# Optimization experiments

Measured on AMD Instinct MI355X. Metric: run time of the kernel, lower is better.

## Reference

```python
import jax, jax.numpy as jnp
import numpy as np

N_LABELS = 48
L = N_LABELS + 2            # labels + stop + start
START = N_LABELS + 1
STOP = N_LABELS
NEG = -10000.0
B, T = 512, 1024


def setup_inputs() -> dict:
    key = jax.random.key(0)
    k1, k2, k3 = jax.random.split(key, 3)
    feats = jax.random.normal(k1, (B, T, L), dtype=jnp.float32)
    lens = jax.random.randint(k2, (B,), 1, T + 1, dtype=jnp.int32)
    transitions = jax.random.normal(k3, (L, L), dtype=jnp.float32)
    return {"feats": feats, "lens": lens, "transitions": transitions}


def reference(feats, lens, transitions):
    # Viterbi decode (module's forward). feats: [B, T, L]
    b, t, l = feats.shape
    vit0 = jnp.full((b, l), NEG, feats.dtype).at[:, START].set(0.0)

    def step(carry, logit):
        vit, c = carry                                   # vit [B,L], c [B]
        scores = vit[:, None, :] + transitions[None, :, :]   # [B, to, from]
        vt_max = scores.max(2)                           # [B, L]
        ptr = scores.argmax(2)                           # [B, L] backpointers
        vit_nxt = vt_max + logit
        vit_new = jnp.where((c > 0)[:, None], vit_nxt, vit)
        # add stop transition exactly when this is the last real timestep
        vit_new = vit_new + jnp.where((c == 1)[:, None], transitions[STOP][None, :], 0.0)
        return (vit_new, c - 1), ptr

    (vit, _), pointers = jax.lax.scan(step, (vit0, lens), jnp.swapaxes(feats, 0, 1))
    scores = vit.max(1)                                  # [B]
    idx = vit.argmax(1)                                  # [B]

    barange = jnp.arange(b)

    def back(i, ptr):
        ni = ptr[barange, i]
        return ni, ni

    _, back_seq = jax.lax.scan(back, idx, pointers, reverse=True)  # back_seq[t] = idx after ptr_t
    # original drops the earliest backtracked index (belongs to the virtual start step)
    paths = jnp.concatenate([back_seq[1:], idx[None]], axis=0).T   # [B, T]
    return scores, paths
```

## Files before the change

### kernel.cpp

```cpp
#include <hip/hip_runtime.h>

typedef unsigned char u8;

#define TT 1024
#define BB 512
#define LL 50
#define STOPI 48
#define STARTI 49
#define NEGV -10000.0f

#define PTR_OFF 4096

#define ROW_ADDS(ROWP, S, TRR)                                                 \
    {                                                                          \
        _Pragma("unroll")                                                      \
        for (int k_ = 0; k_ < 13; ++k_) {                                      \
            const float4 q_ = *(const float4*)((ROWP) + 4 * k_);               \
            const int j_ = 4 * k_;                                             \
            (S)[j_ + 0] = q_.x + (TRR)[j_ + 0];                                \
            (S)[j_ + 1] = q_.y + (TRR)[j_ + 1];                                \
            if (j_ + 2 < LL) (S)[j_ + 2] = q_.z + (TRR)[j_ + 2];               \
            if (j_ + 3 < LL) (S)[j_ + 3] = q_.w + (TRR)[j_ + 3];               \
        }                                                                      \
    }

#define MAX50(S, M)                                                            \
    {                                                                          \
        float r0_[17];                                                         \
        _Pragma("unroll")                                                      \
        for (int k_ = 0; k_ < 16; ++k_)                                        \
            r0_[k_] = fmaxf(fmaxf((S)[3*k_], (S)[3*k_+1]), (S)[3*k_+2]);       \
        r0_[16] = fmaxf((S)[48], (S)[49]);                                     \
        float r1_[6];                                                          \
        _Pragma("unroll")                                                      \
        for (int k_ = 0; k_ < 5; ++k_)                                         \
            r1_[k_] = fmaxf(fmaxf(r0_[3*k_], r0_[3*k_+1]), r0_[3*k_+2]);       \
        r1_[5] = fmaxf(r0_[15], r0_[16]);                                      \
        (M) = fmaxf(fmaxf(fmaxf(r1_[0], r1_[1]), r1_[2]),                      \
                    fmaxf(fmaxf(r1_[3], r1_[4]), r1_[5]));                     \
    }

#define ARGMAX50(S, BI)                                                        \
    {                                                                          \
        float b0_=-3.4e38f, b1_=-3.4e38f, b2_=-3.4e38f, b3_=-3.4e38f;          \
        int   i0_=0, i1_=13, i2_=26, i3_=39;                                   \
        _Pragma("unroll")                                                      \
        for (int j_=0;  j_<13; ++j_){ const float v_=(S)[j_]; if (v_>b0_){b0_=v_;i0_=j_;} } \
        _Pragma("unroll")                                                      \
        for (int j_=13; j_<26; ++j_){ const float v_=(S)[j_]; if (v_>b1_){b1_=v_;i1_=j_;} } \
        _Pragma("unroll")                                                      \
        for (int j_=26; j_<39; ++j_){ const float v_=(S)[j_]; if (v_>b2_){b2_=v_;i2_=j_;} } \
        _Pragma("unroll")                                                      \
        for (int j_=39; j_<50; ++j_){ const float v_=(S)[j_]; if (v_>b3_){b3_=v_;i3_=j_;} } \
        if (b1_>b0_){b0_=b1_;i0_=i1_;}                                         \
        if (b2_>b0_){b0_=b2_;i0_=i2_;}                                         \
        if (b3_>b0_){b0_=b3_;i0_=i3_;}                                         \
        (BI) = i0_;                                                            \
    }

#define PROCESS_GROUP(BASE)                                                    \
    {                                                                          \
        if (!have && (BASE) + 3 > len) {                                       \
            const float* rowp_ = &ring[len & 15][0];                           \
            float s_[LL];                                                      \
            ROW_ADDS(rowp_, s_, trr)                                           \
            ARGMAX50(s_, cidx)                                                 \
            have = true;                                                       \
        }                                                                      \
        unsigned pk_ = 0;                                                      \
        _Pragma("unroll 1")                                                    \
        for (int r_ = 0; r_ < 4; ++r_) {                                       \
            const int t_ = (BASE) + r_;                                        \
            int idx_;                                                          \
            if (t_ <= len) {                                                   \
                const float* rowp_ = &ring[t_ & 15][0];                        \
                float s_[LL];                                                  \
                ROW_ADDS(rowp_, s_, trr)                                       \
                ARGMAX50(s_, idx_)                                             \
            } else {                                                           \
                idx_ = cidx;                                                   \
            }                                                                  \
            pk_ |= (unsigned)idx_ << (8 * r_);                                 \
        }                                                                      \
        if (lane < LL) *(unsigned*)(pt + (BASE)) = pk_;                        \
    }

__global__ __launch_bounds__(192, 2) void viterbi_fused(
    const float* __restrict__ feats, const int* __restrict__ lens,
    const float* __restrict__ trans, float* __restrict__ out_scores,
    int* __restrict__ idx_ws, u8* __restrict__ ptr_ws)
{
    const int b    = blockIdx.x;
    const int tid  = threadIdx.x;
    const int lane = tid & 63;
    const int w    = __builtin_amdgcn_readfirstlane(tid >> 6);
    const int row  = (lane < LL) ? lane : (LL - 1);

    __shared__ float ring[16][64];

    float trr[LL];
#pragma unroll
    for (int j = 0; j < LL; ++j) trr[j] = trans[row * LL + j];
    const int len = lens[b];

    if (w == 0) {
        const float tr_stop = trans[STOPI * LL + row];
        float vit = (lane == STARTI) ? 0.0f : NEGV;
        const float* fb = feats + (size_t)b * (TT * LL);

        float f[8];
#pragma unroll
        for (int i = 0; i < 8; ++i) f[i] = fb[i * LL + row];

        for (int it = 0; it < 128; ++it) {
#pragma unroll
            for (int i = 0; i < 8; ++i) {
                const int t = (it << 3) + i;
                float* rowp = &ring[t & 15][0];
                if (t <= len) {
                    if (lane < LL) rowp[lane] = vit;
                }
                if (t < len) {
                    float s[LL];
                    ROW_ADDS(rowp, s, trr)
                    float m; MAX50(s, m)
                    float nv = m + f[i];
                    if (t == len - 1) nv += tr_stop;
                    vit = nv;
                    int tp = t + 8; if (tp > TT - 1) tp = TT - 1;
                    f[i] = fb[(size_t)tp * LL + row];
                }
            }
            asm volatile("s_waitcnt lgkmcnt(0)" ::: "memory");
            __builtin_amdgcn_s_barrier();
            asm volatile("" ::: "memory");
        }

        float m = -3.4e38f; int mi = 0;
#pragma unroll
        for (int j = 0; j < LL; ++j) {
            float sv = __int_as_float(__builtin_amdgcn_readlane(__float_as_int(vit), j));
            if (sv > m) { m = sv; mi = j; }
        }
        if (lane == 0) { out_scores[b] = m; idx_ws[b] = mi; }
    } else {
        u8* pt = ptr_ws + (size_t)b * (TT * LL) + (size_t)row * TT;
        int  cidx = 0;
        bool have = false;

        for (int it = 0; it < 128; ++it) {
            if (it > 0) {
                const int base = ((it - 1) << 3) + ((w - 1) << 2);
                PROCESS_GROUP(base)
            }
            asm volatile("s_waitcnt lgkmcnt(0)" ::: "memory");
            __builtin_amdgcn_s_barrier();
            asm volatile("" ::: "memory");
        }
        {
            const int base = (127 << 3) + ((w - 1) << 2);
            PROCESS_GROUP(base)
        }
    }
}

#define LSW(S, T) (((S) << 10) + ((T) ^ (((S) & 31) << 2)))

__global__ __launch_bounds__(64) void viterbi_bwd(
    const int* __restrict__ idx_ws, const u8* __restrict__ ptr_ws,
    float* __restrict__ out_paths)
{
    const int b = blockIdx.x;
    const int lane = threadIdx.x;

    __shared__ u8 lptr[TT * LL];
    __shared__ u8 maps[32 * LL];
    __shared__ int entries[33];

    {
        const unsigned* src = (const unsigned*)(ptr_ws + (size_t)b * TT * LL);
        unsigned* dst = (unsigned*)lptr;
        for (int i = lane; i < (TT * LL) / 4; i += 64) {
            const int to = i >> 8;
            const int t4 = i & 255;
            dst[(to << 8) + (t4 ^ (to & 31))] = src[i];
        }
    }
    __syncthreads();

    {
        int st[25], tt[25], cidx[25];
#pragma unroll
        for (int k = 0; k < 25; ++k) {
            int ww = k * 64 + lane;
            int c = ww / 50;
            int l = ww - c * 50;
            st[k] = l;
            tt[k] = c * 32 + 31;
            cidx[k] = c * 50 + l;
        }
        for (int j = 0; j < 32; ++j) {
#pragma unroll
            for (int k = 0; k < 25; ++k) {
                st[k] = lptr[LSW(st[k], tt[k])];
                tt[k] -= 1;
            }
        }
#pragma unroll
        for (int k = 0; k < 25; ++k) maps[cidx[k]] = (u8)st[k];
    }
    __syncthreads();

    const int idx = idx_ws[b];

    if (lane == 0) {
        int i = idx;
        for (int c = 31; c >= 0; --c) {
            entries[c + 1] = i;
            i = maps[c * 50 + i];
        }
        entries[0] = i;
    }
    __syncthreads();

    float* po = out_paths + (size_t)b * TT;
    if (lane < 32) {
        const int c = lane;
        int s = entries[c + 1];
        for (int j = 0; j < 32; ++j) {
            int t = c * 32 + 31 - j;
            int ni = lptr[LSW(s, t)];
            if (t > 0) po[t - 1] = (float)ni;
            s = ni;
        }
    }
    if (lane == 0) po[TT - 1] = (float)idx;
}

extern "C" void kernel_launch(void* const* d_in, const int* in_sizes, int n_in,
                              void* d_out, int out_size, void* d_ws, size_t ws_size,
                              hipStream_t stream) {
    const float* feats = (const float*)d_in[0];
    const int*   lens  = (const int*)d_in[1];
    const float* trans = (const float*)d_in[2];

    float* scores = (float*)d_out;
    float* paths  = scores + BB;

    int* idx_ws = (int*)d_ws;
    u8*  ptr_ws = (u8*)d_ws + PTR_OFF;

    viterbi_fused<<<BB, 192, 0, stream>>>(feats, lens, trans, scores, idx_ws, ptr_ws);
    viterbi_bwd<<<BB, 64, 0, stream>>>(idx_ws, ptr_ws, paths);
}
```

Before: 570.2 us.

## Split forward Viterbi into max-only recurrence and parallel backpointer kernel

Replaces the fused kernel, where one wave ran the recurrence and two waves computed argmax backpointers in lockstep through an LDS ring and barriers. The new first kernel uses a single wave per batch that runs only the max recurrence, broadcasting values with readlane instead of LDS, stops at each sequence's length, and stores every timestep's viterbi vector to global workspace. A second, fully parallel kernel then recomputes the argmax for each 8-timestep chunk from the stored vectors, with no serial dependency. This removes barriers and argmax work from the serial critical path, at the cost of a large extra global write and read of the viterbi states and one more kernel launch.

```diff
diff --git a/kernel.cpp b/kernel.cpp
--- a/kernel.cpp
+++ b/kernel.cpp
@@ -9,20 +9,9 @@
 #define STARTI 49
 #define NEGV -10000.0f
 
-#define PTR_OFF 4096
-
-#define ROW_ADDS(ROWP, S, TRR)                                                 \
-    {                                                                          \
-        _Pragma("unroll")                                                      \
-        for (int k_ = 0; k_ < 13; ++k_) {                                      \
-            const float4 q_ = *(const float4*)((ROWP) + 4 * k_);               \
-            const int j_ = 4 * k_;                                             \
-            (S)[j_ + 0] = q_.x + (TRR)[j_ + 0];                                \
-            (S)[j_ + 1] = q_.y + (TRR)[j_ + 1];                                \
-            if (j_ + 2 < LL) (S)[j_ + 2] = q_.z + (TRR)[j_ + 2];               \
-            if (j_ + 3 < LL) (S)[j_ + 3] = q_.w + (TRR)[j_ + 3];               \
-        }                                                                      \
-    }
+#define PTR_OFF   4096
+#define PTR_BYTES ((size_t)BB * TT * LL)
+#define VIT_OFF   (PTR_OFF + PTR_BYTES)
 
 #define MAX50(S, M)                                                            \
     {                                                                          \
@@ -40,128 +29,140 @@
                     fmaxf(fmaxf(r1_[3], r1_[4]), r1_[5]));                     \
     }
 
-#define ARGMAX50(S, BI)                                                        \
-    {                                                                          \
-        float b0_=-3.4e38f, b1_=-3.4e38f, b2_=-3.4e38f, b3_=-3.4e38f;          \
-        int   i0_=0, i1_=13, i2_=26, i3_=39;                                   \
-        _Pragma("unroll")                                                      \
-        for (int j_=0;  j_<13; ++j_){ const float v_=(S)[j_]; if (v_>b0_){b0_=v_;i0_=j_;} } \
-        _Pragma("unroll")                                                      \
-        for (int j_=13; j_<26; ++j_){ const float v_=(S)[j_]; if (v_>b1_){b1_=v_;i1_=j_;} } \
-        _Pragma("unroll")                                                      \
-        for (int j_=26; j_<39; ++j_){ const float v_=(S)[j_]; if (v_>b2_){b2_=v_;i2_=j_;} } \
-        _Pragma("unroll")                                                      \
-        for (int j_=39; j_<50; ++j_){ const float v_=(S)[j_]; if (v_>b3_){b3_=v_;i3_=j_;} } \
-        if (b1_>b0_){b0_=b1_;i0_=i1_;}                                         \
-        if (b2_>b0_){b0_=b2_;i0_=i2_;}                                         \
-        if (b3_>b0_){b0_=b3_;i0_=i3_;}                                         \
-        (BI) = i0_;                                                            \
-    }
-
-#define PROCESS_GROUP(BASE)                                                    \
-    {                                                                          \
-        if (!have && (BASE) + 3 > len) {                                       \
-            const float* rowp_ = &ring[len & 15][0];                           \
-            float s_[LL];                                                      \
-            ROW_ADDS(rowp_, s_, trr)                                           \
-            ARGMAX50(s_, cidx)                                                 \
-            have = true;                                                       \
-        }                                                                      \
-        unsigned pk_ = 0;                                                      \
-        _Pragma("unroll 1")                                                    \
-        for (int r_ = 0; r_ < 4; ++r_) {                                       \
-            const int t_ = (BASE) + r_;                                        \
-            int idx_;                                                          \
-            if (t_ <= len) {                                                   \
-                const float* rowp_ = &ring[t_ & 15][0];                        \
-                float s_[LL];                                                  \
-                ROW_ADDS(rowp_, s_, trr)                                       \
-                ARGMAX50(s_, idx_)                                             \
-            } else {                                                           \
-                idx_ = cidx;                                                   \
-            }                                                                  \
-            pk_ |= (unsigned)idx_ << (8 * r_);                                 \
-        }                                                                      \
-        if (lane < LL) *(unsigned*)(pt + (BASE)) = pk_;                        \
-    }
-
-__global__ __launch_bounds__(192, 2) void viterbi_fused(
+__global__ __launch_bounds__(64, 1) void viterbi_max(
     const float* __restrict__ feats, const int* __restrict__ lens,
     const float* __restrict__ trans, float* __restrict__ out_scores,
-    int* __restrict__ idx_ws, u8* __restrict__ ptr_ws)
+    int* __restrict__ idx_ws, float* __restrict__ vit_ws)
 {
     const int b    = blockIdx.x;
+    const int lane = threadIdx.x;
+    if (lane >= LL) return;
+
+    float trr[LL];
+#pragma unroll
+    for (int j = 0; j < LL; ++j) trr[j] = trans[lane * LL + j];
+#pragma unroll
+    for (int j = 0; j < LL; ++j) asm("" : "+v"(trr[j]));
+    const float tr_stop = trans[STOPI * LL + lane];
+    const int len = lens[b];
+
+    float vit = (lane == STARTI) ? 0.0f : NEGV;
+
+    const float* fb  = feats  + (size_t)b * (TT * LL);
+    float*       vst = vit_ws + (size_t)b * (TT * LL);
+
+    float f[8];
+#pragma unroll
+    for (int i = 0; i < 8; ++i) f[i] = fb[i * LL + lane];
+
+    const int nfull = len >> 3;
+    for (int it = 0; it < nfull; ++it) {
+#pragma unroll
+        for (int i = 0; i < 8; ++i) {
+            const int t = (it << 3) + i;
+            vst[(size_t)t * LL + lane] = vit;
+            float x[LL];
+#pragma unroll
+            for (int j = 0; j < LL; ++j)
+                x[j] = __int_as_float(__builtin_amdgcn_readlane(
+                           __float_as_int(vit), j)) + trr[j];
+            float m; MAX50(x, m)
+            vit = m + f[i];
+            int tp = t + 8; if (tp > TT - 1) tp = TT - 1;
+            f[i] = fb[(size_t)tp * LL + lane];
+        }
+    }
+
+    for (int t = nfull << 3; t < len; ++t) {
+        vst[(size_t)t * LL + lane] = vit;
+        float x[LL];
+#pragma unroll
+        for (int j = 0; j < LL; ++j)
+            x[j] = __int_as_float(__builtin_amdgcn_readlane(
+                       __float_as_int(vit), j)) + trr[j];
+        float m; MAX50(x, m)
+        vit = m + fb[(size_t)t * LL + lane];
+    }
+
+    vit += tr_stop;
+
+    if (len < TT) vst[(size_t)len * LL + lane] = vit;
+
+    float m = -3.4e38f; int mi = 0;
+#pragma unroll
+    for (int j = 0; j < LL; ++j) {
+        float s = __int_as_float(__builtin_amdgcn_readlane(__float_as_int(vit), j));
+        if (s > m) { m = s; mi = j; }
+    }
+    if (lane == 0) { out_scores[b] = m; idx_ws[b] = mi; }
+}
+
+#define K2ROW(T, IDX)                                                          \
+    {                                                                          \
+        const int r_ = ((T) < len) ? (T) : len;                                \
+        if (r_ != prev_r) {                                                    \
+            prev_r = r_;                                                       \
+            const float v_ = vbase[(size_t)r_ * LL + lane];                    \
+            float x_[LL];                                                      \
+            _Pragma("unroll")                                                  \
+            for (int j_ = 0; j_ < LL; ++j_)                                    \
+                x_[j_] = __int_as_float(__builtin_amdgcn_readlane(             \
+                             __float_as_int(v_), j_)) + trr[j_];               \
+            float m_; MAX50(x_, m_)                                            \
+            int ia_ = 63, ib_ = 63, ic_ = 63, id_ = 63;                        \
+            _Pragma("unroll")                                                  \
+            for (int j_ = 0; j_ < 48; j_ += 4) {                               \
+                { int c_ = (x_[j_+0]==m_) ? (j_+0) : 63; ia_ = c_<ia_?c_:ia_; }\
+                { int c_ = (x_[j_+1]==m_) ? (j_+1) : 63; ib_ = c_<ib_?c_:ib_; }\
+                { int c_ = (x_[j_+2]==m_) ? (j_+2) : 63; ic_ = c_<ic_?c_:ic_; }\
+                { int c_ = (x_[j_+3]==m_) ? (j_+3) : 63; id_ = c_<id_?c_:id_; }\
+            }                                                                  \
+            { int c_ = (x_[48]==m_) ? 48 : 63; ia_ = c_<ia_?c_:ia_; }          \
+            { int c_ = (x_[49]==m_) ? 49 : 63; ib_ = c_<ib_?c_:ib_; }          \
+            const int m0_ = ia_ < ib_ ? ia_ : ib_;                             \
+            const int m1_ = ic_ < id_ ? ic_ : id_;                             \
+            cached = m0_ < m1_ ? m0_ : m1_;                                    \
+        }                                                                      \
+        (IDX) = cached;                                                        \
+    }
+
+__global__ __launch_bounds__(256, 2) void viterbi_ptr(
+    const int* __restrict__ lens, const float* __restrict__ trans,
+    const float* __restrict__ vit_ws, u8* __restrict__ ptr_ws)
+{
     const int tid  = threadIdx.x;
     const int lane = tid & 63;
-    const int w    = __builtin_amdgcn_readfirstlane(tid >> 6);
-    const int row  = (lane < LL) ? lane : (LL - 1);
-
-    __shared__ float ring[16][64];
+    if (lane >= LL) return;
+    const int wid = (blockIdx.x << 2) | (tid >> 6);
+    const int b   = wid >> 7;
+    const int t0  = (wid & 127) << 3;
 
     float trr[LL];
 #pragma unroll
-    for (int j = 0; j < LL; ++j) trr[j] = trans[row * LL + j];
+    for (int j = 0; j < LL; ++j) trr[j] = trans[lane * LL + j];
+#pragma unroll
+    for (int j = 0; j < LL; ++j) asm("" : "+v"(trr[j]));
     const int len = lens[b];
 
-    if (w == 0) {
-        const float tr_stop = trans[STOPI * LL + row];
-        float vit = (lane == STARTI) ? 0.0f : NEGV;
-        const float* fb = feats + (size_t)b * (TT * LL);
-
-        float f[8];
-#pragma unroll
-        for (int i = 0; i < 8; ++i) f[i] = fb[i * LL + row];
-
-        for (int it = 0; it < 128; ++it) {
-#pragma unroll
-            for (int i = 0; i < 8; ++i) {
-                const int t = (it << 3) + i;
-                float* rowp = &ring[t & 15][0];
-                if (t <= len) {
-                    if (lane < LL) rowp[lane] = vit;
-                }
-                if (t < len) {
-                    float s[LL];
-                    ROW_ADDS(rowp, s, trr)
-                    float m; MAX50(s, m)
-                    float nv = m + f[i];
-                    if (t == len - 1) nv += tr_stop;
-                    vit = nv;
-                    int tp = t + 8; if (tp > TT - 1) tp = TT - 1;
-                    f[i] = fb[(size_t)tp * LL + row];
-                }
-            }
-            asm volatile("s_waitcnt lgkmcnt(0)" ::: "memory");
-            __builtin_amdgcn_s_barrier();
-            asm volatile("" ::: "memory");
-        }
-
-        float m = -3.4e38f; int mi = 0;
-#pragma unroll
-        for (int j = 0; j < LL; ++j) {
-            float sv = __int_as_float(__builtin_amdgcn_readlane(__float_as_int(vit), j));
-            if (sv > m) { m = sv; mi = j; }
-        }
-        if (lane == 0) { out_scores[b] = m; idx_ws[b] = mi; }
-    } else {
-        u8* pt = ptr_ws + (size_t)b * (TT * LL) + (size_t)row * TT;
-        int  cidx = 0;
-        bool have = false;
-
-        for (int it = 0; it < 128; ++it) {
-            if (it > 0) {
-                const int base = ((it - 1) << 3) + ((w - 1) << 2);
-                PROCESS_GROUP(base)
-            }
-            asm volatile("s_waitcnt lgkmcnt(0)" ::: "memory");
-            __builtin_amdgcn_s_barrier();
-            asm volatile("" ::: "memory");
-        }
-        {
-            const int base = (127 << 3) + ((w - 1) << 2);
-            PROCESS_GROUP(base)
-        }
-    }
+    const float* vbase = vit_ws + (size_t)b * (TT * LL);
+    u8* pt = ptr_ws + (size_t)b * (TT * LL) + (size_t)lane * TT;
+
+    int prev_r = -1, cached = 0;
+
+    unsigned pk0 = 0;
+#pragma unroll 1
+    for (int g = 0; g < 4; ++g) {
+        int idx; K2ROW(t0 + g, idx)
+        pk0 |= (unsigned)idx << (8 * g);
+    }
+    unsigned pk1 = 0;
+#pragma unroll 1
+    for (int g = 4; g < 8; ++g) {
+        int idx; K2ROW(t0 + g, idx)
+        pk1 |= (unsigned)idx << (8 * (g - 4));
+    }
+    *(unsigned*)(pt + t0)     = pk0;
+    *(unsigned*)(pt + t0 + 4) = pk1;
 }
 
 #define LSW(S, T) (((S) << 10) + ((T) ^ (((S) & 31) << 2)))
@@ -192,9 +193,9 @@
         int st[25], tt[25], cidx[25];
 #pragma unroll
         for (int k = 0; k < 25; ++k) {
-            int ww = k * 64 + lane;
-            int c = ww / 50;
-            int l = ww - c * 50;
+            int w = k * 64 + lane;
+            int c = w / 50;
+            int l = w - c * 50;
             st[k] = l;
             tt[k] = c * 32 + 31;
             cidx[k] = c * 50 + l;
@@ -247,9 +248,11 @@
     float* scores = (float*)d_out;
     float* paths  = scores + BB;
 
-    int* idx_ws = (int*)d_ws;
-    u8*  ptr_ws = (u8*)d_ws + PTR_OFF;
-
-    viterbi_fused<<<BB, 192, 0, stream>>>(feats, lens, trans, scores, idx_ws, ptr_ws);
+    int*   idx_ws = (int*)d_ws;
+    u8*    ptr_ws = (u8*)d_ws + PTR_OFF;
+    float* vit_ws = (float*)((u8*)d_ws + VIT_OFF);
+
+    viterbi_max<<<BB, 64, 0, stream>>>(feats, lens, trans, scores, idx_ws, vit_ws);
+    viterbi_ptr<<<(BB * 128) / 4, 256, 0, stream>>>(lens, trans, vit_ws, ptr_ws);
     viterbi_bwd<<<BB, 64, 0, stream>>>(idx_ws, ptr_ws, paths);
 }
```

Measured after the change: 626.5 us. 9.9% more time.
